# Kernel optimization log

Measured on AMD Instinct MI355X. Metric: run time of the kernel, lower is better.

## Reference

```python
import jax, jax.numpy as jnp
import numpy as np

N = 100000   # nodes
E = 1600000  # edges
IN = 32      # in_channels
H = 64       # hidden_channels
L = 16       # latent_dim
G = 64       # graphs in batch


def setup_inputs() -> dict:
    key = jax.random.key(0)
    ks = jax.random.split(key, 20)
    def w(k, shape, fan):
        return jax.random.normal(k, shape, jnp.float32) * (1.0 / np.sqrt(fan))
    inp = {}
    inp["x"] = jax.random.normal(ks[0], (N, IN), jnp.float32)
    inp["edge_index"] = jax.random.randint(ks[1], (2, E), 0, N)
    inp["batch"] = jnp.sort(jax.random.randint(ks[2], (N,), 0, G))
    # encoder GCN convs: in->h, h->h, h->h
    inp["W_enc0"] = w(ks[3], (IN, H), IN); inp["b_enc0"] = jnp.zeros((H,), jnp.float32)
    inp["W_enc1"] = w(ks[4], (H, H), H);   inp["b_enc1"] = jnp.zeros((H,), jnp.float32)
    inp["W_enc2"] = w(ks[5], (H, H), H);   inp["b_enc2"] = jnp.zeros((H,), jnp.float32)
    # latent projection and decoder projection
    inp["W_proj"] = w(ks[6], (H, L), H);   inp["b_proj"] = jnp.zeros((L,), jnp.float32)
    inp["W_dec_proj"] = w(ks[7], (L, H), L); inp["b_dec_proj"] = jnp.zeros((H,), jnp.float32)
    # decoder GCN convs: h->h, h->in
    inp["W_dec0"] = w(ks[8], (H, H), H);   inp["b_dec0"] = jnp.zeros((H,), jnp.float32)
    inp["W_dec1"] = w(ks[9], (H, IN), H);  inp["b_dec1"] = jnp.zeros((IN,), jnp.float32)
    return inp


def gcn_conv(x, W, b, src, dst, dinv):
    xw = x @ W                                   # [N, out]
    coef = (dinv[src] * dinv[dst])[:, None]      # [E, 1]
    out = jax.ops.segment_sum(xw[src] * coef, dst, num_segments=N)
    out = out + xw * (dinv * dinv)[:, None]      # self-loop contribution
    return out + b


def reference(x, edge_index, batch,
              W_enc0, b_enc0, W_enc1, b_enc1, W_enc2, b_enc2,
              W_proj, b_proj, W_dec_proj, b_dec_proj,
              W_dec0, b_dec0, W_dec1, b_dec1):
    src, dst = edge_index[0], edge_index[1]
    # degree with self-loops (computed on target nodes, PyG default)
    deg = jax.ops.segment_sum(jnp.ones((E,), jnp.float32), dst, num_segments=N) + 1.0
    dinv = jax.lax.rsqrt(deg)
    # encoder (eval mode: dropout is identity)
    h = jax.nn.relu(gcn_conv(x, W_enc0, b_enc0, src, dst, dinv))
    h = jax.nn.relu(gcn_conv(h, W_enc1, b_enc1, src, dst, dinv))
    h = jax.nn.relu(gcn_conv(h, W_enc2, b_enc2, src, dst, dinv))
    # global mean pool over graph ids
    sums = jax.ops.segment_sum(h, batch, num_segments=G)
    cnt = jax.ops.segment_sum(jnp.ones((N,), jnp.float32), batch, num_segments=G)
    g = sums / jnp.maximum(cnt, 1.0)[:, None]    # [G, H]
    z = g @ W_proj + b_proj                      # [G, L]
    # decoder: broadcast z back to nodes, project, two GCN convs
    d = jax.nn.relu(z[batch] @ W_dec_proj + b_dec_proj)
    d = jax.nn.relu(gcn_conv(d, W_dec0, b_dec0, src, dst, dinv))
    x_recon = gcn_conv(d, W_dec1, b_dec1, src, dst, dinv)
    return (x_recon, z)
```

## Files before the change

### kernel.cpp

```cpp
#include <hip/hip_runtime.h>
#include <hip/hip_bf16.h>

typedef unsigned long long u64;

static constexpr int IN_CH  = 32;
static constexpr int HID    = 64;
static constexpr int LAT    = 16;
static constexpr int NGRAPH = 64;
static constexpr int KB_CSR  = 24;


__device__ inline void add4(float4& a, const float4& b) {
    a.x += b.x; a.y += b.y; a.z += b.z; a.w += b.w;
}


__global__ __launch_bounds__(256) void bhist_kernel(const int* __restrict__ ei,
                                                    int* __restrict__ bh, int E) {
    __shared__ int lh[256];
    lh[threadIdx.x] = 0;
    __syncthreads();
    int base = blockIdx.x * 2048;
    #pragma unroll
    for (int j = 0; j < 8; j++) {
        int idx = base + j * 256 + threadIdx.x;
        if (idx < E) atomicAdd(&lh[ei[E + idx] >> 9], 1);
    }
    __syncthreads();
    if (lh[threadIdx.x]) atomicAdd(&bh[threadIdx.x], lh[threadIdx.x]);
}


__global__ __launch_bounds__(256) void bin_kernel(
        const int* __restrict__ ei, const int* __restrict__ bh,
        int* __restrict__ gcur, u64* __restrict__ sout, int E) {
    __shared__ int lhist[256], lscan[256], lcur[256], gbase[256], bbaseL[256];
    __shared__ u64 sbuf[2048];
    int tid = threadIdx.x;
    lhist[tid] = 0;
    {
        int v = bh[tid];
        lscan[tid] = v;
        for (int off = 1; off < 256; off <<= 1) {
            __syncthreads();
            int x = (tid >= off) ? lscan[tid - off] : 0;
            __syncthreads();
            lscan[tid] += x;
        }
        __syncthreads();
        bbaseL[tid] = lscan[tid] - v;
    }
    __syncthreads();
    int base = blockIdx.x * 2048;
    int cnt = min(2048, E - base);
    int myb[8]; u64 myp[8];
    #pragma unroll
    for (int j = 0; j < 8; j++) {
        int idx = base + j * 256 + tid;
        myb[j] = -1;
        if (idx < E) {
            int key = ei[E + idx], val = ei[idx];
            int b = key >> 9;
            myb[j] = b;
            myp[j] = ((u64)(unsigned)key << 32) | (unsigned)val;
            atomicAdd(&lhist[b], 1);
        }
    }
    __syncthreads();
    int v = lhist[tid];
    lscan[tid] = v;
    for (int off = 1; off < 256; off <<= 1) {
        __syncthreads();
        int x = (tid >= off) ? lscan[tid - off] : 0;
        __syncthreads();
        lscan[tid] += x;
    }
    __syncthreads();
    int excl = lscan[tid] - v;
    __syncthreads();
    lscan[tid] = excl;
    lcur[tid] = excl;
    __syncthreads();
    #pragma unroll
    for (int j = 0; j < 8; j++) {
        if (myb[j] >= 0) {
            int pos = atomicAdd(&lcur[myb[j]], 1);
            sbuf[pos] = myp[j];
        }
    }
    gbase[tid] = v ? atomicAdd(&gcur[tid], v) : 0;
    __syncthreads();
    for (int i = tid; i < cnt; i += 256) {
        u64 p = sbuf[i];
        int b = (int)(p >> 41);
        sout[bbaseL[b] + gbase[b] + (i - lscan[b])] = p;
    }
}


__global__ __launch_bounds__(256) void degb_kernel(
        const u64* __restrict__ staged, const int* __restrict__ bh,
        const int* __restrict__ batch,
        int* __restrict__ rank, int* __restrict__ perm, int* __restrict__ cnt2,
        int* __restrict__ rowptr2, float* __restrict__ dinvR,
        float2* __restrict__ pgR, int* __restrict__ bbase, int N, int E) {
    __shared__ int sc[256];
    __shared__ int ldeg[512], lrank[512], degS[512], psum[512];
    __shared__ int kcur[256];
    __shared__ int s0s, s1s;
    int b = blockIdx.x, tid = threadIdx.x;
    {
        int bv = bh[tid];
        sc[tid] = bv;
        for (int off = 1; off < 256; off <<= 1) {
            __syncthreads();
            int x = (tid >= off) ? sc[tid - off] : 0;
            __syncthreads();
            sc[tid] += x;
        }
        __syncthreads();
        if (tid == b) { s0s = sc[tid] - bv; s1s = sc[tid]; }
    }
    ldeg[tid] = 0; ldeg[tid + 256] = 0;
    degS[tid] = 0; degS[tid + 256] = 0;
    kcur[tid] = 0;
    __syncthreads();
    int s0 = s0s, s1 = s1s;
    int base = b << 9;
    for (int i = s0 + tid; i < s1; i += 256)
        atomicAdd(&ldeg[(int)(__builtin_nontemporal_load(&staged[i]) >> 32) - base], 1);
    __syncthreads();
    int k = N - base; k = k < 0 ? 0 : (k > 512 ? 512 : k);
    #pragma unroll
    for (int j = 0; j < 2; j++) {
        int t = tid + j * 256;
        if (t < k) atomicAdd(&kcur[min(ldeg[t], 255)], 1);
    }
    __syncthreads();
    {
        int hv = kcur[tid];
        sc[tid] = hv;
        for (int off = 1; off < 256; off <<= 1) {
            __syncthreads();
            int x = (tid >= off) ? sc[tid - off] : 0;
            __syncthreads();
            sc[tid] += x;
        }
        __syncthreads();
        kcur[tid] = sc[tid] - hv;
    }
    __syncthreads();
    #pragma unroll
    for (int j = 0; j < 2; j++) {
        int t = tid + j * 256;
        if (t < k) lrank[t] = atomicAdd(&kcur[min(ldeg[t], 255)], 1);
    }
    __syncthreads();
    #pragma unroll
    for (int j = 0; j < 2; j++) {
        int t = tid + j * 256;
        if (t < k) degS[lrank[t]] = ldeg[t];
    }
    __syncthreads();
    {
        int v0 = degS[2 * tid], v1 = degS[2 * tid + 1];
        int T = v0 + v1;
        sc[tid] = T;
        for (int off = 1; off < 256; off <<= 1) {
            __syncthreads();
            int x = (tid >= off) ? sc[tid - off] : 0;
            __syncthreads();
            sc[tid] += x;
        }
        __syncthreads();
        int ex = sc[tid] - T;
        psum[2 * tid] = ex;
        psum[2 * tid + 1] = ex + v0;
    }
    __syncthreads();
    #pragma unroll
    for (int j = 0; j < 2; j++) {
        int t = tid + j * 256;
        if (t < k) {
            int n = base + t;
            int d = ldeg[t], lr = lrank[t];
            int r = base + lr;
            rank[n] = r;
            perm[r] = n;
            cnt2[r] = d;
            rowptr2[r] = s0 + psum[lr];
            float dv = rsqrtf((float)d + 1.0f);
            dinvR[r] = dv;
            pgR[r] = make_float2(dv, __int_as_float(batch[n]));
        }
    }
    if (tid == 0) {
        bbase[b] = s0;
        if (b == 255) bbase[256] = E;
    }
}


__global__ __launch_bounds__(256) void csr_kernel(
        const u64* __restrict__ staged, const int* __restrict__ bbase,
        const int* __restrict__ rank, const int* __restrict__ rowptr2,
        int* __restrict__ cur, int* __restrict__ col) {
    int bucket = blockIdx.x & 255;
    int k = blockIdx.x >> 8;
    int s0 = bbase[bucket], s1 = bbase[bucket + 1];
    for (int i = s0 + k * 256 + threadIdx.x; i < s1; i += 256 * KB_CSR) {
        u64 p = __builtin_nontemporal_load(&staged[i]);
        int dst = (int)(p >> 32);
        int src = (int)(p & 0xffffffffu);
        int rd = rank[dst];
        int pos = rowptr2[rd] + atomicAdd(&cur[rd], 1);
        col[pos] = rank[src];
    }
}


__global__ void slice_x_kernel(const float* __restrict__ x, const int* __restrict__ perm,
                               const float* __restrict__ dinvR,
                               float* __restrict__ xs, int N) {
    int idx = blockIdx.x * 256 + threadIdx.x;
    if (idx >= N * 2) return;
    int r = idx >> 1, h = idx & 1;
    int sl = blockIdx.y;
    int n = perm[r];
    float4 v = ((const float4*)x)[(size_t)n * 8 + sl * 2 + h];
    float dn = dinvR[r];
    v.x *= dn; v.y *= dn; v.z *= dn; v.w *= dn;
    ((float4*)(xs + (size_t)sl * N * 8))[idx] = v;
}


template <int C, bool ADD_BIAS, bool OUT_ROWMAJOR>
__global__ __launch_bounds__(256) void agg_kernel(
        const float* __restrict__ in, float* __restrict__ out,
        const int* __restrict__ rowptr2, const int* __restrict__ cnt2,
        const int* __restrict__ col, const float* __restrict__ dinvR,
        const int* __restrict__ perm, const float* __restrict__ bias, int N) {
    constexpr int NSL = C / 8;
    int sl = blockIdx.x % NSL;
    int chunk = blockIdx.x / NSL;
    int slot = threadIdx.x >> 1, h = threadIdx.x & 1;
    int r = chunk * 128 + slot;
    if (r >= N) return;
    const float4* inS = (const float4*)(in + (size_t)sl * N * 8);
    int start = rowptr2[r], m = cnt2[r];
    const int* cp = col + start;
    float4 acc = inS[(size_t)r * 2 + h];
    int i = 0;
    for (; i + 8 <= m; i += 8) {
        int s0 = cp[i], s1 = cp[i+1], s2 = cp[i+2], s3 = cp[i+3];
        int s4 = cp[i+4], s5 = cp[i+5], s6 = cp[i+6], s7 = cp[i+7];
        float4 v0 = inS[(size_t)s0*2+h], v1 = inS[(size_t)s1*2+h];
        float4 v2 = inS[(size_t)s2*2+h], v3 = inS[(size_t)s3*2+h];
        float4 v4 = inS[(size_t)s4*2+h], v5 = inS[(size_t)s5*2+h];
        float4 v6 = inS[(size_t)s6*2+h], v7 = inS[(size_t)s7*2+h];
        add4(v0, v1); add4(v2, v3); add4(v4, v5); add4(v6, v7);
        add4(v0, v2); add4(v4, v6);
        add4(acc, v0); add4(acc, v4);
    }
    if (i + 4 <= m) {
        int s0 = cp[i], s1 = cp[i+1], s2 = cp[i+2], s3 = cp[i+3];
        float4 v0 = inS[(size_t)s0*2+h], v1 = inS[(size_t)s1*2+h];
        float4 v2 = inS[(size_t)s2*2+h], v3 = inS[(size_t)s3*2+h];
        add4(v0, v1); add4(v2, v3); add4(v0, v2);
        add4(acc, v0);
        i += 4;
    }
    for (; i < m; ++i) {
        int c = cp[i];
        add4(acc, inS[(size_t)c * 2 + h]);
    }
    float dn = dinvR[r];
    acc.x *= dn; acc.y *= dn; acc.z *= dn; acc.w *= dn;
    if (ADD_BIAS) {
        float4 b4 = ((const float4*)bias)[sl * 2 + h];
        add4(acc, b4);
    }
    if (OUT_ROWMAJOR) ((float4*)out)[(size_t)perm[r] * (C / 4) + sl * 2 + h] = acc;
    else ((float4*)(out + (size_t)sl * N * 8))[(size_t)r * 2 + h] = acc;
}


__global__ __launch_bounds__(256) void gagg_kernel(
        const float* __restrict__ dg, const float2* __restrict__ pgR,
        const int* __restrict__ rowptr2, const int* __restrict__ cnt2,
        const int* __restrict__ col, float* __restrict__ out, int N) {
    __shared__ float dgL[NGRAPH * 68];
    for (int i = threadIdx.x; i < NGRAPH * 64; i += 256)
        dgL[(i >> 6) * 68 + (i & 63)] = dg[i];
    __syncthreads();
    int slot = threadIdx.x >> 1, e = threadIdx.x & 1;
    int r = blockIdx.x * 128 + slot;
    if (r >= N) return;
    const float4* dgL4 = (const float4*)dgL;
    int start = rowptr2[r], m = cnt2[r];
    const int* cp = col + start;
    float2 ps = pgR[r];
    float dn = ps.x;
    int gs = __float_as_int(ps.y);
    float4 acc[8];
    {
        const float4* rp = dgL4 + gs * 17 + e * 8;
        #pragma unroll
        for (int j = 0; j < 8; ++j) {
            float4 v = rp[j];
            acc[j] = make_float4(dn * v.x, dn * v.y, dn * v.z, dn * v.w);
        }
    }
    int i = 0;
    for (; i + 2 <= m; i += 2) {
        int c0 = cp[i], c1 = cp[i + 1];
        float2 p0 = pgR[c0], p1 = pgR[c1];
        const float4* r0 = dgL4 + __float_as_int(p0.y) * 17 + e * 8;
        const float4* r1 = dgL4 + __float_as_int(p1.y) * 17 + e * 8;
        float w0 = p0.x, w1 = p1.x;
        #pragma unroll
        for (int j = 0; j < 8; ++j) {
            float4 v0 = r0[j], v1 = r1[j];
            acc[j].x += w0 * v0.x + w1 * v1.x;
            acc[j].y += w0 * v0.y + w1 * v1.y;
            acc[j].z += w0 * v0.z + w1 * v1.z;
            acc[j].w += w0 * v0.w + w1 * v1.w;
        }
    }
    if (i < m) {
        int c0 = cp[i];
        float2 p0 = pgR[c0];
        const float4* r0 = dgL4 + __float_as_int(p0.y) * 17 + e * 8;
        float w0 = p0.x;
        #pragma unroll
        for (int j = 0; j < 8; ++j) {
            float4 v0 = r0[j];
            acc[j].x += w0 * v0.x; acc[j].y += w0 * v0.y;
            acc[j].z += w0 * v0.z; acc[j].w += w0 * v0.w;
        }
    }
    #pragma unroll
    for (int k = 0; k < 4; ++k) {
        #pragma unroll
        for (int jj = 0; jj < 2; ++jj) {
            float4 v = acc[k * 2 + jj];
            v.x *= dn; v.y *= dn; v.z *= dn; v.w *= dn;
            ((float4*)(out + (size_t)(4 * e + k) * N * 8))[(size_t)r * 2 + jj] = v;
        }
    }
}


template <int CIN, int COUT, bool RELU, bool BIAS, bool SCALE, bool OUT_ROWMAJOR>
__global__ __launch_bounds__(256) void gemm_kernel(
        const float* __restrict__ in, const float* __restrict__ W,
        const float* __restrict__ b, const float* __restrict__ dinvR,
        const int* __restrict__ perm, float* __restrict__ out, int N) {
    constexpr int NPB = 256 / COUT;
    constexpr int K4 = CIN / 4;
    __shared__ float4 xsh[NPB * K4];
    int r  = threadIdx.x / COUT;
    int co = threadIdx.x % COUT;
    float w[CIN];
    #pragma unroll
    for (int k = 0; k < CIN; ++k) w[k] = W[k * COUT + co];
    float bsv = BIAS ? b[co] : 0.f;
    int ngroups = (N + NPB - 1) / NPB;
    for (int grp = blockIdx.x; grp < ngroups; grp += gridDim.x) {
        int base = grp * NPB;
        __syncthreads();
        for (int i = threadIdx.x; i < NPB * K4; i += 256) {
            int rr = i / K4, k4 = i % K4;
            int n = base + rr;
            float4 v = make_float4(0.f, 0.f, 0.f, 0.f);
            if (n < N) v = ((const float4*)(in + (size_t)(k4 >> 1) * N * 8))[(size_t)n * 2 + (k4 & 1)];
            xsh[i] = v;
        }
        __syncthreads();
        int n = base + r;
        if (n < N) {
            float acc = bsv;
            #pragma unroll
            for (int k4 = 0; k4 < K4; ++k4) {
                float4 xv = xsh[r * K4 + k4];
                acc += xv.x * w[4 * k4] + xv.y * w[4 * k4 + 1]
                     + xv.z * w[4 * k4 + 2] + xv.w * w[4 * k4 + 3];
            }
            if (RELU) acc = fmaxf(acc, 0.f);
            if (SCALE) acc *= dinvR[n];
            if (OUT_ROWMAJOR) out[(size_t)perm[n] * COUT + co] = acc;
            else out[(size_t)(co >> 3) * N * 8 + (size_t)n * 8 + (co & 7)] = acc;
        }
    }
}


__global__ __launch_bounds__(256) void pool_kernel(
        const float* __restrict__ h, const int* __restrict__ batch,
        float* __restrict__ sums, int* __restrict__ cntb, int N) {
    const int CHUNK = 512;
    int chunkStart = blockIdx.x * CHUNK;
    int c = threadIdx.x & 63;
    int r = threadIdx.x >> 6;
    int curg = -1;
    float acc = 0.f;
    int cnt = 0;
    int end = chunkStart + CHUNK;
    if (end > N) end = N;
    for (int n = chunkStart + r; n < end; n += 4) {
        int g = batch[n];
        if (g != curg) {
            if (curg >= 0) {
                atomicAdd(&sums[curg * 64 + c], acc);
                if (c == 0) atomicAdd(&cntb[curg], cnt);
            }
            curg = g; acc = 0.f; cnt = 0;
        }
        acc += h[(size_t)n * 64 + c];
        cnt++;
    }
    if (curg >= 0) {
        atomicAdd(&sums[curg * 64 + c], acc);
        if (c == 0) atomicAdd(&cntb[curg], cnt);
    }
}


__global__ __launch_bounds__(1024) void latent_kernel(
        const float* __restrict__ sums, const int* __restrict__ cntb,
        const float* __restrict__ Wp, const float* __restrict__ bp,
        const float* __restrict__ Wd, const float* __restrict__ bd,
        float* __restrict__ z_out, float* __restrict__ dg) {
    __shared__ float zl[NGRAPH * LAT];
    int t = threadIdx.x;
    {
        int g = t / LAT, l = t % LAT;
        float cf = (float)cntb[g];
        float inv = 1.0f / fmaxf(cf, 1.0f);
        float acc = bp[l];
        #pragma unroll
        for (int k = 0; k < HID; k++) acc += sums[g * HID + k] * inv * Wp[k * LAT + l];
        zl[t] = acc;
        z_out[t] = acc;
    }
    __syncthreads();
    #pragma unroll
    for (int i = 0; i < 4; i++) {
        int idx = t + i * 1024;
        int g = idx >> 6, c = idx & 63;
        float acc = bd[c];
        #pragma unroll
        for (int l = 0; l < LAT; l++) acc += zl[g * LAT + l] * Wd[l * HID + c];
        dg[idx] = fmaxf(acc, 0.f);
    }
}


extern "C" void kernel_launch(void* const* d_in, const int* in_sizes, int n_in,
                              void* d_out, int out_size, void* d_ws, size_t ws_size,
                              hipStream_t stream) {
    const float* x          = (const float*)d_in[0];
    const int*   ei         = (const int*)d_in[1];
    const int*   batch      = (const int*)d_in[2];
    const float* W_enc0     = (const float*)d_in[3];
    const float* b_enc0     = (const float*)d_in[4];
    const float* W_enc1     = (const float*)d_in[5];
    const float* b_enc1     = (const float*)d_in[6];
    const float* W_enc2     = (const float*)d_in[7];
    const float* b_enc2     = (const float*)d_in[8];
    const float* W_proj     = (const float*)d_in[9];
    const float* b_proj     = (const float*)d_in[10];
    const float* W_dec_proj = (const float*)d_in[11];
    const float* b_dec_proj = (const float*)d_in[12];
    const float* W_dec0     = (const float*)d_in[13];
    const float* b_dec0     = (const float*)d_in[14];
    const float* W_dec1     = (const float*)d_in[15];
    const float* b_dec1     = (const float*)d_in[16];

    const int N = in_sizes[0] / IN_CH;
    const int E = in_sizes[1] / 2;

    char* ws = (char*)d_ws;
    size_t off = 0;
    auto alloc = [&](size_t bytes) {
        void* p = ws + off;
        off += (bytes + 255) & ~(size_t)255;
        return p;
    };
    float* A       = (float*)alloc((size_t)N * HID * 4);
    float* B       = (float*)alloc((size_t)N * HID * 4);
    float* XS      = (float*)alloc((size_t)N * IN_CH * 4);
    int*   col     = (int*)  alloc((size_t)E * 4);
    int*   cnt2    = (int*)  alloc((size_t)N * 4);
    int*   rowptr2 = (int*)  alloc((size_t)(N + 1) * 4);
    int*   perm    = (int*)  alloc((size_t)N * 4);
    int*   rank    = (int*)  alloc((size_t)N * 4);
    float* dinvR   = (float*)alloc((size_t)N * 4);
    float2* pgR    = (float2*)alloc((size_t)N * 8);
    int*   bbase   = (int*)  alloc(257 * 4);
    char* zbase = ws + off;
    int*   cursor  = (int*)  alloc((size_t)N * 4);
    int*   bh      = (int*)  alloc(256 * 4);
    int*   gcurD   = (int*)  alloc(256 * 4);
    float* sums    = (float*)alloc((size_t)NGRAPH * HID * 4);
    int*   cntb    = (int*)  alloc((size_t)NGRAPH * 4);
    size_t zbytes = (size_t)((ws + off) - zbase);
    float* dg      = (float*)alloc((size_t)NGRAPH * HID * 4);

    u64* staged1 = (u64*)XS;

    float* x_recon = (float*)d_out;
    float* z_out   = (float*)d_out + (size_t)N * IN_CH;

    hipMemsetAsync(zbase, 0, zbytes, stream);

    int ebins = (E + 2047) / 2048;
    int chunks = (N + 127) / 128;

    bhist_kernel<<<ebins, 256, 0, stream>>>(ei, bh, E);
    bin_kernel<<<ebins, 256, 0, stream>>>(ei, bh, gcurD, staged1, E);
    degb_kernel<<<256, 256, 0, stream>>>(staged1, bh, batch, rank, perm, cnt2,
                                         rowptr2, dinvR, pgR, bbase, N, E);
    csr_kernel<<<256 * KB_CSR, 256, 0, stream>>>(staged1, bbase, rank, rowptr2, cursor, col);

    {
        dim3 g((N * 2 + 255) / 256, IN_CH / 8);
        slice_x_kernel<<<g, 256, 0, stream>>>(x, perm, dinvR, XS, N);
    }

    agg_kernel<IN_CH, false, false><<<chunks * 4, 256, 0, stream>>>(
        XS, A, rowptr2, cnt2, col, dinvR, perm, nullptr, N);
    gemm_kernel<IN_CH, HID, true, true, true, false><<<2048, 256, 0, stream>>>(
        A, W_enc0, b_enc0, dinvR, perm, B, N);
    agg_kernel<HID, false, false><<<chunks * 8, 256, 0, stream>>>(
        B, A, rowptr2, cnt2, col, dinvR, perm, nullptr, N);
    gemm_kernel<HID, HID, true, true, true, false><<<2048, 256, 0, stream>>>(
        A, W_enc1, b_enc1, dinvR, perm, B, N);
    agg_kernel<HID, false, false><<<chunks * 8, 256, 0, stream>>>(
        B, A, rowptr2, cnt2, col, dinvR, perm, nullptr, N);
    gemm_kernel<HID, HID, true, true, false, true><<<2048, 256, 0, stream>>>(
        A, W_enc2, b_enc2, dinvR, perm, B, N);

    pool_kernel<<<(N + 511) / 512, 256, 0, stream>>>(B, batch, sums, cntb, N);
    latent_kernel<<<1, 1024, 0, stream>>>(sums, cntb, W_proj, b_proj, W_dec_proj, b_dec_proj, z_out, dg);

    gagg_kernel<<<chunks, 256, 0, stream>>>(dg, pgR, rowptr2, cnt2, col, A, N);
    gemm_kernel<HID, HID, true, true, false, false><<<2048, 256, 0, stream>>>(
        A, W_dec0, b_dec0, dinvR, perm, B, N);
    gemm_kernel<HID, IN_CH, false, false, true, false><<<2048, 256, 0, stream>>>(
        B, W_dec1, nullptr, dinvR, perm, A, N);
    agg_kernel<IN_CH, true, true><<<chunks * 4, 256, 0, stream>>>(
        A, x_recon, rowptr2, cnt2, col, dinvR, perm, b_dec1, N);
}
```

Measured before the change: 686.2 us.

## Fuse decoder GEMMs and interleave aggregation block-to-chunk mapping

```diff
diff --git a/kernel.cpp b/kernel.cpp
--- a/kernel.cpp
+++ b/kernel.cpp
@@ -8,6 +8,7 @@
 static constexpr int LAT    = 16;
 static constexpr int NGRAPH = 64;
 static constexpr int KB_CSR  = 24;
+static constexpr int CPB     = 4;
 
 
 __device__ inline void add4(float4& a, const float4& b) {
@@ -239,10 +240,12 @@
         const float* __restrict__ in, float* __restrict__ out,
         const int* __restrict__ rowptr2, const int* __restrict__ cnt2,
         const int* __restrict__ col, const float* __restrict__ dinvR,
-        const int* __restrict__ perm, const float* __restrict__ bias, int N) {
+        const int* __restrict__ perm, const float* __restrict__ bias,
+        int nbk, int N) {
     constexpr int NSL = C / 8;
     int sl = blockIdx.x % NSL;
-    int chunk = blockIdx.x / NSL;
+    int o  = blockIdx.x / NSL;
+    int chunk = (o % nbk) * CPB + (o / nbk);
     int slot = threadIdx.x >> 1, h = threadIdx.x & 1;
     int r = chunk * 128 + slot;
     if (r >= N) return;
@@ -288,13 +291,15 @@
 __global__ __launch_bounds__(256) void gagg_kernel(
         const float* __restrict__ dg, const float2* __restrict__ pgR,
         const int* __restrict__ rowptr2, const int* __restrict__ cnt2,
-        const int* __restrict__ col, float* __restrict__ out, int N) {
+        const int* __restrict__ col, float* __restrict__ out, int nbk, int N) {
     __shared__ float dgL[NGRAPH * 68];
     for (int i = threadIdx.x; i < NGRAPH * 64; i += 256)
         dgL[(i >> 6) * 68 + (i & 63)] = dg[i];
     __syncthreads();
     int slot = threadIdx.x >> 1, e = threadIdx.x & 1;
-    int r = blockIdx.x * 128 + slot;
+    int o = blockIdx.x;
+    int chunk = (o % nbk) * CPB + (o / nbk);
+    int r = chunk * 128 + slot;
     if (r >= N) return;
     const float4* dgL4 = (const float4*)dgL;
     int start = rowptr2[r], m = cnt2[r];
@@ -390,6 +395,62 @@
             if (SCALE) acc *= dinvR[n];
             if (OUT_ROWMAJOR) out[(size_t)perm[n] * COUT + co] = acc;
             else out[(size_t)(co >> 3) * N * 8 + (size_t)n * 8 + (co & 7)] = acc;
+        }
+    }
+}
+
+
+__global__ __launch_bounds__(256) void gemm2_kernel(
+        const float* __restrict__ in, const float* __restrict__ W0,
+        const float* __restrict__ b0, const float* __restrict__ W1,
+        const float* __restrict__ dinvR, float* __restrict__ out, int N) {
+    constexpr int NPB = 4;
+    __shared__ float4 xsh[NPB * 16];
+    __shared__ float t1sh[NPB * 65];
+    __shared__ float w1sh[HID * IN_CH];
+    int tid = threadIdx.x;
+    int r  = tid >> 6;
+    int co = tid & 63;
+    float w0[HID];
+    #pragma unroll
+    for (int k = 0; k < HID; ++k) w0[k] = W0[k * HID + co];
+    float b0v = b0[co];
+    for (int i = tid; i < HID * IN_CH; i += 256) w1sh[i] = W1[i];
+    int r2  = tid >> 5;
+    int co2 = tid & 31;
+    int ngroups = (N + NPB - 1) / NPB;
+    for (int grp = blockIdx.x; grp < ngroups; grp += gridDim.x) {
+        int base = grp * NPB;
+        __syncthreads();
+        if (tid < NPB * 16) {
+            int rr = tid >> 4, k4 = tid & 15;
+            int n = base + rr;
+            float4 v = make_float4(0.f, 0.f, 0.f, 0.f);
+            if (n < N) v = ((const float4*)(in + (size_t)(k4 >> 1) * N * 8))[(size_t)n * 2 + (k4 & 1)];
+            xsh[tid] = v;
+        }
+        __syncthreads();
+        {
+            float acc = b0v;
+            #pragma unroll
+            for (int k4 = 0; k4 < 16; ++k4) {
+                float4 xv = xsh[r * 16 + k4];
+                acc += xv.x * w0[4 * k4] + xv.y * w0[4 * k4 + 1]
+                     + xv.z * w0[4 * k4 + 2] + xv.w * w0[4 * k4 + 3];
+            }
+            t1sh[r * 65 + co] = fmaxf(acc, 0.f);
+        }
+        __syncthreads();
+        if (r2 < NPB) {
+            int n = base + r2;
+            if (n < N) {
+                float acc = 0.f;
+                #pragma unroll
+                for (int k = 0; k < HID; ++k)
+                    acc += t1sh[r2 * 65 + k] * w1sh[k * IN_CH + co2];
+                acc *= dinvR[n];
+                out[(size_t)(co2 >> 3) * N * 8 + (size_t)n * 8 + (co2 & 7)] = acc;
+            }
         }
     }
 }
@@ -515,7 +576,8 @@
     hipMemsetAsync(zbase, 0, zbytes, stream);
 
     int ebins = (E + 2047) / 2048;
-    int chunks = (N + 127) / 128;
+    int nbk = (N + 511) >> 9;
+    int chunksI = nbk * CPB;
 
     bhist_kernel<<<ebins, 256, 0, stream>>>(ei, bh, E);
     bin_kernel<<<ebins, 256, 0, stream>>>(ei, bh, gcurD, staged1, E);
@@ -528,27 +590,24 @@
         slice_x_kernel<<<g, 256, 0, stream>>>(x, perm, dinvR, XS, N);
     }
 
-    agg_kernel<IN_CH, false, false><<<chunks * 4, 256, 0, stream>>>(
-        XS, A, rowptr2, cnt2, col, dinvR, perm, nullptr, N);
+    agg_kernel<IN_CH, false, false><<<chunksI * 4, 256, 0, stream>>>(
+        XS, A, rowptr2, cnt2, col, dinvR, perm, nullptr, nbk, N);
     gemm_kernel<IN_CH, HID, true, true, true, false><<<2048, 256, 0, stream>>>(
         A, W_enc0, b_enc0, dinvR, perm, B, N);
-    agg_kernel<HID, false, false><<<chunks * 8, 256, 0, stream>>>(
-        B, A, rowptr2, cnt2, col, dinvR, perm, nullptr, N);
+    agg_kernel<HID, false, false><<<chunksI * 8, 256, 0, stream>>>(
+        B, A, rowptr2, cnt2, col, dinvR, perm, nullptr, nbk, N);
     gemm_kernel<HID, HID, true, true, true, false><<<2048, 256, 0, stream>>>(
         A, W_enc1, b_enc1, dinvR, perm, B, N);
-    agg_kernel<HID, false, false><<<chunks * 8, 256, 0, stream>>>(
-        B, A, rowptr2, cnt2, col, dinvR, perm, nullptr, N);
+    agg_kernel<HID, false, false><<<chunksI * 8, 256, 0, stream>>>(
+        B, A, rowptr2, cnt2, col, dinvR, perm, nullptr, nbk, N);
     gemm_kernel<HID, HID, true, true, false, true><<<2048, 256, 0, stream>>>(
         A, W_enc2, b_enc2, dinvR, perm, B, N);
 
     pool_kernel<<<(N + 511) / 512, 256, 0, stream>>>(B, batch, sums, cntb, N);
     latent_kernel<<<1, 1024, 0, stream>>>(sums, cntb, W_proj, b_proj, W_dec_proj, b_dec_proj, z_out, dg);
 
-    gagg_kernel<<<chunks, 256, 0, stream>>>(dg, pgR, rowptr2, cnt2, col, A, N);
-    gemm_kernel<HID, HID, true, true, false, false><<<2048, 256, 0, stream>>>(
-        A, W_dec0, b_dec0, dinvR, perm, B, N);
-    gemm_kernel<HID, IN_CH, false, false, true, false><<<2048, 256, 0, stream>>>(
-        B, W_dec1, nullptr, dinvR, perm, A, N);
-    agg_kernel<IN_CH, true, true><<<chunks * 4, 256, 0, stream>>>(
-        A, x_recon, rowptr2, cnt2, col, dinvR, perm, b_dec1, N);
-}
+    gagg_kernel<<<chunksI, 256, 0, stream>>>(dg, pgR, rowptr2, cnt2, col, A, nbk, N);
+    gemm2_kernel<<<2048, 256, 0, stream>>>(A, W_dec0, b_dec0, W_dec1, dinvR, B, N);
+    agg_kernel<IN_CH, true, true><<<chunksI * 4, 256, 0, stream>>>(
+        B, x_recon, rowptr2, cnt2, col, dinvR, perm, b_dec1, nbk, N);
+}
```

After: 638.7 us. 6.9% less time.
